# Performance work log

Measured on AMD Instinct MI355X. Metric: run time of the kernel, lower is better.

The kernel has to match this reference:

```python
import jax, jax.numpy as jnp
import numpy as np

K = 12  # kNN neighbors (includes self, as in PyG knn(x, x, k))
EPS = 1e-5


def bn(h, g, b):
    # Training-mode BatchNorm over all axes except the last (feature) axis.
    ax = tuple(range(h.ndim - 1))
    m = h.mean(axis=ax, keepdims=True)
    v = h.var(axis=ax, keepdims=True)  # biased variance, as BN uses
    return g * (h - m) * jax.lax.rsqrt(v + EPS) + b


def edge_conv(x, W1, b1, g, be, W2, b2):
    # x: [B, N, C] -> [B, N, H]. Dynamic kNN graph in feature space per graph.
    d2 = jnp.sum(x * x, axis=-1)                                  # [B, N]
    dist = d2[:, :, None] + d2[:, None, :] - 2.0 * jnp.einsum('bic,bjc->bij', x, x)
    _, idx = jax.lax.top_k(-dist, K)                              # [B, N, K]
    xj = jnp.take_along_axis(x[:, None, :, :], idx[:, :, :, None], axis=2)  # [B,N,K,C]
    xi = jnp.broadcast_to(x[:, :, None, :], xj.shape)
    e = jnp.concatenate([xi, xj - xi], axis=-1)                   # [B,N,K,2C]
    h = jax.nn.relu(bn(jnp.einsum('bnkc,ch->bnkh', e, W1) + b1, g, be))
    h = jnp.einsum('bnkh,ho->bnko', h, W2) + b2
    return h.mean(axis=2)                                         # mean aggr over K


def setup_inputs() -> dict:
    key = jax.random.key(0)
    ks = jax.random.split(key, 8)
    B, N, C, H, Hf, O = 32, 1024, 3, 64, 32, 2
    s = 0.1
    return {
        'x': jax.random.normal(ks[0], (B, N, C), jnp.float32),
        'w0a': jax.random.normal(ks[1], (2 * C, H), jnp.float32) * s,
        'b0a': jnp.zeros((H,), jnp.float32),
        'g0': jnp.ones((H,), jnp.float32),
        'be0': jnp.zeros((H,), jnp.float32),
        'w0b': jax.random.normal(ks[2], (H, H), jnp.float32) * s,
        'b0b': jnp.zeros((H,), jnp.float32),
        'wa': jax.random.normal(ks[3], (3, 2 * H, H), jnp.float32) * s,
        'ba': jnp.zeros((3, H), jnp.float32),
        'ga': jnp.ones((3, H), jnp.float32),
        'bea': jnp.zeros((3, H), jnp.float32),
        'wb': jax.random.normal(ks[4], (3, H, H), jnp.float32) * s,
        'bb': jnp.zeros((3, H), jnp.float32),
        'wf1': jax.random.normal(ks[5], (H, Hf), jnp.float32) * s,
        'bf1': jnp.zeros((Hf,), jnp.float32),
        'gf': jnp.ones((Hf,), jnp.float32),
        'bef': jnp.zeros((Hf,), jnp.float32),
        'wf2': jax.random.normal(ks[6], (Hf, O), jnp.float32) * s,
        'bf2': jnp.zeros((O,), jnp.float32),
    }


def reference(x, w0a, b0a, g0, be0, w0b, b0b, wa, ba, ga, bea, wb, bb,
              wf1, bf1, gf, bef, wf2, bf2):
    # Layer 0: input channels = 3
    h = edge_conv(x, w0a, b0a, g0, be0, w0b, b0b)
    # Layers 1..3: input channels = hidden
    for i in range(3):
        h = edge_conv(h, wa[i], ba[i], ga[i], bea[i], wb[i], bb[i])
    pooled = h.mean(axis=1)  # global_mean_pool over nodes -> [B, H]
    z = jax.nn.relu(bn(pooled @ wf1 + bf1, gf, bef))
    return z @ wf2 + bf2     # [B, 2]
```

## Files before the change

kernel.cpp:

```cpp
#include <hip/hip_runtime.h>
#include <cstddef>

#define BATCH 32
#define NPTS  1024
#define K_NN  12
#define HID   64
#define BN_EPS 1e-5f

typedef short bf16x8 __attribute__((ext_vector_type(8)));
typedef float f32x4 __attribute__((ext_vector_type(4)));

__device__ __forceinline__ unsigned long long dkey(float dval, int j) {
  int di = __float_as_int(dval);
  unsigned m = (unsigned)(di >> 31) | 0x80000000u;
  unsigned u = (unsigned)di ^ m;
  return ((unsigned long long)u << 32) | (unsigned)j;
}

__device__ __forceinline__ void cas_u64(unsigned long long &a, unsigned long long &b) {
  unsigned long long x = a, y = b;
  bool c = y < x;
  a = c ? y : x;
  b = c ? x : y;
}

__device__ __forceinline__ void sort16_u64(unsigned long long (&k)[16]) {
  cas_u64(k[0],k[1]);  cas_u64(k[2],k[3]);  cas_u64(k[4],k[5]);  cas_u64(k[6],k[7]);
  cas_u64(k[8],k[9]);  cas_u64(k[10],k[11]); cas_u64(k[12],k[13]); cas_u64(k[14],k[15]);
  cas_u64(k[0],k[2]);  cas_u64(k[1],k[3]);  cas_u64(k[4],k[6]);  cas_u64(k[5],k[7]);
  cas_u64(k[8],k[10]); cas_u64(k[9],k[11]); cas_u64(k[12],k[14]); cas_u64(k[13],k[15]);
  cas_u64(k[1],k[2]);  cas_u64(k[5],k[6]);  cas_u64(k[9],k[10]); cas_u64(k[13],k[14]);
  cas_u64(k[0],k[4]);  cas_u64(k[1],k[5]);  cas_u64(k[2],k[6]);  cas_u64(k[3],k[7]);
  cas_u64(k[8],k[12]); cas_u64(k[9],k[13]); cas_u64(k[10],k[14]); cas_u64(k[11],k[15]);
  cas_u64(k[2],k[4]);  cas_u64(k[3],k[5]);  cas_u64(k[10],k[12]); cas_u64(k[11],k[13]);
  cas_u64(k[1],k[2]);  cas_u64(k[3],k[4]);  cas_u64(k[5],k[6]);
  cas_u64(k[9],k[10]); cas_u64(k[11],k[12]); cas_u64(k[13],k[14]);
  cas_u64(k[0],k[8]);  cas_u64(k[1],k[9]);  cas_u64(k[2],k[10]); cas_u64(k[3],k[11]);
  cas_u64(k[4],k[12]); cas_u64(k[5],k[13]); cas_u64(k[6],k[14]); cas_u64(k[7],k[15]);
  cas_u64(k[4],k[8]);  cas_u64(k[5],k[9]);  cas_u64(k[6],k[10]); cas_u64(k[7],k[11]);
  cas_u64(k[2],k[4]);  cas_u64(k[3],k[5]);  cas_u64(k[6],k[8]);  cas_u64(k[7],k[9]);
  cas_u64(k[10],k[12]); cas_u64(k[11],k[13]);
  cas_u64(k[1],k[2]);  cas_u64(k[3],k[4]);  cas_u64(k[5],k[6]);  cas_u64(k[7],k[8]);
  cas_u64(k[9],k[10]); cas_u64(k[11],k[12]); cas_u64(k[13],k[14]);
}

__device__ __forceinline__ void merge12_u64(unsigned long long (&L)[12],
                                            const unsigned long long* S) {
#pragma unroll
  for (int i = 0; i < 12; ++i) {
    unsigned long long s = S[11 - i];
    L[i] = L[i] < s ? L[i] : s;
  }
  cas_u64(L[0],L[8]);  cas_u64(L[1],L[9]);  cas_u64(L[2],L[10]); cas_u64(L[3],L[11]);
  cas_u64(L[4],L[8]);  cas_u64(L[5],L[9]);  cas_u64(L[6],L[10]); cas_u64(L[7],L[11]);
  cas_u64(L[0],L[2]);  cas_u64(L[1],L[3]);  cas_u64(L[4],L[6]);  cas_u64(L[5],L[7]);
  cas_u64(L[8],L[10]); cas_u64(L[9],L[11]);
  cas_u64(L[0],L[1]);  cas_u64(L[2],L[3]);  cas_u64(L[4],L[5]);  cas_u64(L[6],L[7]);
  cas_u64(L[8],L[9]);  cas_u64(L[10],L[11]);
}

__global__ __launch_bounds__(512, 2) void knn64_mfma_kernel(
    const unsigned short* __restrict__ xh, const unsigned short* __restrict__ xm,
    const unsigned short* __restrict__ xl, const float* __restrict__ d2,
    int* __restrict__ idx,
    const float* __restrict__ hxi, const float* __restrict__ hxj,
    float* __restrict__ partial) {
  const int b    = blockIdx.y;
  const int lane = threadIdx.x & 63;
  const int wv_u = __builtin_amdgcn_readfirstlane(threadIdx.x >> 6);
  const int i0   = blockIdx.x * 64;
  const size_t bbase = (size_t)b * NPTS;
  const float* d2b = d2 + bbase;

  constexpr int NE = 8 * K_NN;
  __shared__ __align__(16) char smem[60416];
  unsigned short* alds = (unsigned short*)smem;
  float* slab = (float*)(smem + 25600 + wv_u * 4352);
  unsigned long long* lk = (unsigned long long*)smem;
  int* jlds = (int*)(smem + 49664);
  float* red1 = (float*)smem;
  float* red2 = (float*)(smem + 2048);

  const int qr = lane >> 4;
  const int lr = lane & 15;

  for (int it = threadIdx.x; it < 1536; it += 512) {
    const int row = it / 24, rem = it % 24, pl = rem >> 3, seg = rem & 7;
    const unsigned short* src = (pl == 0) ? xh : ((pl == 1) ? xm : xl);
    *(bf16x8*)(alds + row * 200 + pl * 64 + seg * 8) =
        *(const bf16x8*)(src + (bbase + i0 + row) * HID + seg * 8);
  }
  __syncthreads();

  unsigned long long L[K_NN];
#pragma unroll
  for (int k = 0; k < K_NN; ++k) L[k] = ~0ULL;

  const int j0 = wv_u * 128;

  bf16x8 Bh0, Bh1, Bm0, Bm1, Bl0, Bl1;
  {
    const size_t brow = (bbase + j0 + lr) * HID;
    Bh0 = *(const bf16x8*)(xh + brow + 0  + qr * 8);
    Bh1 = *(const bf16x8*)(xh + brow + 32 + qr * 8);
    Bm0 = *(const bf16x8*)(xm + brow + 0  + qr * 8);
    Bm1 = *(const bf16x8*)(xm + brow + 32 + qr * 8);
    Bl0 = *(const bf16x8*)(xl + brow + 0  + qr * 8);
    Bl1 = *(const bf16x8*)(xl + brow + 32 + qr * 8);
  }

#pragma unroll 1
  for (int chunk = 0; chunk < 8; ++chunk) {
    const int jb = j0 + chunk * 16;
    const bf16x8 bh0 = Bh0, bh1 = Bh1, bm0 = Bm0, bm1 = Bm1, bl0 = Bl0, bl1 = Bl1;

    f32x4 acc[4];
#pragma unroll
    for (int isub = 0; isub < 4; ++isub) acc[isub] = f32x4{0.f, 0.f, 0.f, 0.f};

#pragma unroll
    for (int isub = 0; isub < 4; ++isub) {
      const int ar = (isub * 16 + lr) * 200;
      bf16x8 Ah0 = *(const bf16x8*)(alds + ar + 0   + qr * 8);
      bf16x8 Ah1 = *(const bf16x8*)(alds + ar + 32  + qr * 8);
      bf16x8 Am0 = *(const bf16x8*)(alds + ar + 64  + qr * 8);
      bf16x8 Am1 = *(const bf16x8*)(alds + ar + 96  + qr * 8);
      bf16x8 Al0 = *(const bf16x8*)(alds + ar + 128 + qr * 8);
      bf16x8 Al1 = *(const bf16x8*)(alds + ar + 160 + qr * 8);
      f32x4 a = acc[isub];
      a = __builtin_amdgcn_mfma_f32_16x16x32_bf16(Ah0, bh0, a, 0, 0, 0);
      a = __builtin_amdgcn_mfma_f32_16x16x32_bf16(Ah1, bh1, a, 0, 0, 0);
      a = __builtin_amdgcn_mfma_f32_16x16x32_bf16(Ah0, bm0, a, 0, 0, 0);
      a = __builtin_amdgcn_mfma_f32_16x16x32_bf16(Ah1, bm1, a, 0, 0, 0);
      a = __builtin_amdgcn_mfma_f32_16x16x32_bf16(Am0, bh0, a, 0, 0, 0);
      a = __builtin_amdgcn_mfma_f32_16x16x32_bf16(Am1, bh1, a, 0, 0, 0);
      a = __builtin_amdgcn_mfma_f32_16x16x32_bf16(Ah0, bl0, a, 0, 0, 0);
      a = __builtin_amdgcn_mfma_f32_16x16x32_bf16(Ah1, bl1, a, 0, 0, 0);
      a = __builtin_amdgcn_mfma_f32_16x16x32_bf16(Al0, bh0, a, 0, 0, 0);
      a = __builtin_amdgcn_mfma_f32_16x16x32_bf16(Al1, bh1, a, 0, 0, 0);
      a = __builtin_amdgcn_mfma_f32_16x16x32_bf16(Am0, bm0, a, 0, 0, 0);
      a = __builtin_amdgcn_mfma_f32_16x16x32_bf16(Am1, bm1, a, 0, 0, 0);
      acc[isub] = a;
    }

    if (chunk < 7) {
      const size_t nrow = (bbase + jb + 16 + lr) * HID;
      Bh0 = *(const bf16x8*)(xh + nrow + 0  + qr * 8);
      Bh1 = *(const bf16x8*)(xh + nrow + 32 + qr * 8);
      Bm0 = *(const bf16x8*)(xm + nrow + 0  + qr * 8);
      Bm1 = *(const bf16x8*)(xm + nrow + 32 + qr * 8);
      Bl0 = *(const bf16x8*)(xl + nrow + 0  + qr * 8);
      Bl1 = *(const bf16x8*)(xl + nrow + 32 + qr * 8);
    }

#pragma unroll
    for (int isub = 0; isub < 4; ++isub)
#pragma unroll
      for (int r = 0; r < 4; ++r)
        slab[(isub * 16 + qr * 4 + r) * 17 + lr] = acc[isub][r];

    unsigned long long S[16];
#pragma unroll
    for (int jj = 0; jj < 16; ++jj) {
      const int j = jb + jj;
      const float dot = slab[lane * 17 + jj];
      const float dval = fmaf(-2.f, dot, d2b[j]);
      S[jj] = dkey(dval, j);
    }
    sort16_u64(S);
    merge12_u64(L, S);
  }

  __syncthreads();
#pragma unroll
  for (int k = 0; k < K_NN; ++k)
    lk[lane * (NE + 1) + wv_u * K_NN + k] = L[k];
  __syncthreads();

  unsigned long long Lm[K_NN];
  if (wv_u < 2) {
    if (wv_u == 0) {
#pragma unroll
      for (int k = 0; k < K_NN; ++k) Lm[k] = L[k];
    } else {
#pragma unroll
      for (int k = 0; k < K_NN; ++k) Lm[k] = lk[lane * (NE + 1) + 4 * K_NN + k];
    }
#pragma unroll 1
    for (int w = 1; w < 4; ++w) {
      unsigned long long M[K_NN];
#pragma unroll
      for (int k = 0; k < K_NN; ++k)
        M[k] = lk[lane * (NE + 1) + (wv_u * 4 + w) * K_NN + k];
      merge12_u64(Lm, M);
    }
  }
  __syncthreads();
  if (wv_u == 1) {
#pragma unroll
    for (int k = 0; k < K_NN; ++k) lk[lane * (NE + 1) + 4 * K_NN + k] = Lm[k];
  }
  __syncthreads();
  if (wv_u == 0) {
    unsigned long long M[K_NN];
#pragma unroll
    for (int k = 0; k < K_NN; ++k) M[k] = lk[lane * (NE + 1) + 4 * K_NN + k];
    merge12_u64(Lm, M);
    int* op = idx + ((size_t)b * NPTS + i0 + lane) * K_NN;
#pragma unroll
    for (int k = 0; k < K_NN; ++k) {
      int jv = (int)(unsigned)(Lm[k] & 0xFFFFFFFFu);
      op[k] = jv;
      jlds[lane * K_NN + k] = jv;
    }
  }
  __syncthreads();

  {
    const float* hxib = hxi + (bbase + i0) * HID;
    const float* hxjb = hxj + bbase * HID;
    float s1 = 0.f, s2 = 0.f;
#pragma unroll 1
    for (int t = 0; t < 8; ++t) {
      const int nl = wv_u * 8 + t;
      const float hv = hxib[(size_t)nl * HID + lane];
      int jj[K_NN];
#pragma unroll
      for (int k = 0; k < K_NN; ++k) jj[k] = jlds[nl * K_NN + k];
      float v[K_NN];
#pragma unroll
      for (int k = 0; k < K_NN; ++k) v[k] = hxjb[(size_t)jj[k] * HID + lane];
#pragma unroll
      for (int k = 0; k < K_NN; ++k) {
        float h = hv + v[k];
        s1 += h;
        s2 = fmaf(h, h, s2);
      }
    }
    red1[wv_u * HID + lane] = s1;
    red2[wv_u * HID + lane] = s2;
  }
  __syncthreads();
  if (threadIdx.x < 128) {
    const int f = threadIdx.x & 63;
    const float* r = (threadIdx.x < 64) ? red1 : red2;
    float a = 0.f;
#pragma unroll
    for (int w = 0; w < 8; ++w) a += r[w * HID + f];
    partial[((size_t)b * 16 + blockIdx.x) * 128 + threadIdx.x] = a;
  }
}

__global__ __launch_bounds__(512, 4) void knn3_kernel(
    const float* __restrict__ x, const float* __restrict__ d2,
    int* __restrict__ idx,
    const float* __restrict__ hxi, const float* __restrict__ hxj,
    float* __restrict__ partial) {
  const int b    = blockIdx.y;
  const int lane = threadIdx.x & 63;
  const int wv_u = __builtin_amdgcn_readfirstlane(threadIdx.x >> 6);
  const int i0   = blockIdx.x * 64;
  const int i    = i0 + lane;
  const size_t bbase = (size_t)b * NPTS;
  const float* xb  = x  + bbase * 3;
  const float* d2b = d2 + bbase;

  __shared__ __align__(16) char smem[27648];
  unsigned long long* buf = (unsigned long long*)smem;
  int* jlds = (int*)(smem + 24576);
  float* red1 = (float*)smem;
  float* red2 = (float*)(smem + 2048);

  float xi0 = xb[(size_t)i * 3 + 0];
  float xi1 = xb[(size_t)i * 3 + 1];
  float xi2v = xb[(size_t)i * 3 + 2];

  unsigned long long L[K_NN];
#pragma unroll
  for (int k = 0; k < K_NN; ++k) L[k] = ~0ULL;

  const int j0 = wv_u * 128;
#pragma unroll 1
  for (int ch = 0; ch < 8; ++ch) {
    unsigned long long S[16];
#pragma unroll
    for (int jj = 0; jj < 16; ++jj) {
      const int j = j0 + ch * 16 + jj;
      const float* xj = xb + (size_t)j * 3;
      const float d2j = d2b[j];
      float dot = fmaf(xi0, xj[0], 0.f);
      dot = fmaf(xi1, xj[1], dot);
      dot = fmaf(xi2v, xj[2], dot);
      S[jj] = dkey(fmaf(-2.f, dot, d2j), j);
    }
    sort16_u64(S);
    merge12_u64(L, S);
  }

  if (wv_u >= 4) {
#pragma unroll
    for (int k = 0; k < K_NN; ++k)
      buf[((wv_u - 4) * 64 + lane) * K_NN + k] = L[k];
  }
  __syncthreads();
  if (wv_u < 4) {
    unsigned long long M[K_NN];
#pragma unroll
    for (int k = 0; k < K_NN; ++k) M[k] = buf[(wv_u * 64 + lane) * K_NN + k];
    merge12_u64(L, M);
  }
  __syncthreads();
  if (wv_u == 2 || wv_u == 3) {
#pragma unroll
    for (int k = 0; k < K_NN; ++k)
      buf[((wv_u - 2) * 64 + lane) * K_NN + k] = L[k];
  }
  __syncthreads();
  if (wv_u < 2) {
    unsigned long long M[K_NN];
#pragma unroll
    for (int k = 0; k < K_NN; ++k) M[k] = buf[(wv_u * 64 + lane) * K_NN + k];
    merge12_u64(L, M);
  }
  __syncthreads();
  if (wv_u == 1) {
#pragma unroll
    for (int k = 0; k < K_NN; ++k) buf[lane * K_NN + k] = L[k];
  }
  __syncthreads();
  if (wv_u == 0) {
    unsigned long long M[K_NN];
#pragma unroll
    for (int k = 0; k < K_NN; ++k) M[k] = buf[lane * K_NN + k];
    merge12_u64(L, M);
    int* op = idx + ((size_t)b * NPTS + i0 + lane) * K_NN;
#pragma unroll
    for (int k = 0; k < K_NN; ++k) {
      int jv = (int)(unsigned)(L[k] & 0xFFFFFFFFu);
      op[k] = jv;
      jlds[lane * K_NN + k] = jv;
    }
  }
  __syncthreads();

  {
    const float* hxib = hxi + (bbase + i0) * HID;
    const float* hxjb2 = hxj + bbase * HID;
    float s1 = 0.f, s2 = 0.f;
#pragma unroll 1
    for (int t = 0; t < 8; ++t) {
      const int nl = wv_u * 8 + t;
      const float hv = hxib[(size_t)nl * HID + lane];
      int jj[K_NN];
#pragma unroll
      for (int k = 0; k < K_NN; ++k) jj[k] = jlds[nl * K_NN + k];
      float v[K_NN];
#pragma unroll
      for (int k = 0; k < K_NN; ++k) v[k] = hxjb2[(size_t)jj[k] * HID + lane];
#pragma unroll
      for (int k = 0; k < K_NN; ++k) {
        float h = hv + v[k];
        s1 += h;
        s2 = fmaf(h, h, s2);
      }
    }
    red1[wv_u * HID + lane] = s1;
    red2[wv_u * HID + lane] = s2;
  }
  __syncthreads();
  if (threadIdx.x < 128) {
    const int f = threadIdx.x & 63;
    const float* r = (threadIdx.x < 64) ? red1 : red2;
    float a = 0.f;
#pragma unroll
    for (int w = 0; w < 8; ++w) a += r[w * HID + f];
    partial[((size_t)b * 16 + blockIdx.x) * 128 + threadIdx.x] = a;
  }
}

__global__ __launch_bounds__(256) void rowgemm2_kernel(
    const float* __restrict__ X, const float* __restrict__ waL,
    const float* __restrict__ biasA,
    float* __restrict__ YA, float* __restrict__ YB) {
  __shared__ float wsa[HID * HID];
  __shared__ float wsb[HID * HID];
  for (int t = threadIdx.x; t < HID * HID; t += 256) {
    float wbv = waL[4096 + t];
    wsa[t] = waL[t] - wbv;
    wsb[t] = wbv;
  }
  __syncthreads();

  const int lane = threadIdx.x & 63;
  const int wv   = threadIdx.x >> 6;
  const int fq   = lane & 15;
  const int rg   = lane >> 4;
  const int r0   = blockIdx.x * 32 + wv * 8 + rg * 2;

  const float4* X4 = (const float4*)X;
  const float4* WA4 = (const float4*)wsa;
  const float4* WB4 = (const float4*)wsb;
  float aA0[4] = {0,0,0,0}, aA1[4] = {0,0,0,0};
  float aB0[4] = {0,0,0,0}, aB1[4] = {0,0,0,0};

#pragma unroll 2
  for (int cq = 0; cq < 16; ++cq) {
    float4 xa = X4[(size_t)r0 * 16 + cq];
    float4 xb_ = X4[(size_t)(r0 + 1) * 16 + cq];
    float ea[4] = {xa.x, xa.y, xa.z, xa.w};
    float eb[4] = {xb_.x, xb_.y, xb_.z, xb_.w};
#pragma unroll
    for (int d = 0; d < 4; ++d) {
      float4 wa4 = WA4[(cq * 4 + d) * 16 + fq];
      float4 wb4 = WB4[(cq * 4 + d) * 16 + fq];
      float wA[4] = {wa4.x, wa4.y, wa4.z, wa4.w};
      float wB[4] = {wb4.x, wb4.y, wb4.z, wb4.w};
#pragma unroll
      for (int k = 0; k < 4; ++k) {
        aA0[k] = fmaf(ea[d], wA[k], aA0[k]);
        aA1[k] = fmaf(eb[d], wA[k], aA1[k]);
        aB0[k] = fmaf(ea[d], wB[k], aB0[k]);
        aB1[k] = fmaf(eb[d], wB[k], aB1[k]);
      }
    }
  }
  float4 b4 = ((const float4*)biasA)[fq];
  float4 oA0{aA0[0] + b4.x, aA0[1] + b4.y, aA0[2] + b4.z, aA0[3] + b4.w};
  float4 oA1{aA1[0] + b4.x, aA1[1] + b4.y, aA1[2] + b4.z, aA1[3] + b4.w};
  float4 oB0{aB0[0], aB0[1], aB0[2], aB0[3]};
  float4 oB1{aB1[0], aB1[1], aB1[2], aB1[3]};
  ((float4*)YA)[(size_t)r0 * 16 + fq] = oA0;
  ((float4*)YA)[(size_t)(r0 + 1) * 16 + fq] = oA1;
  ((float4*)YB)[(size_t)r0 * 16 + fq] = oB0;
  ((float4*)YB)[(size_t)(r0 + 1) * 16 + fq] = oB1;
}

__global__ __launch_bounds__(256) void dual3_kernel(
    const float* __restrict__ x, const float* __restrict__ w0a,
    const float* __restrict__ b1,
    float* __restrict__ hxi, float* __restrict__ hxj,
    float* __restrict__ d2out) {
  __shared__ float Cs[3 * HID], Bs[3 * HID], bs[HID];
  for (int t = threadIdx.x; t < 3 * HID; t += 256) {
    float bv = w0a[192 + t];
    Cs[t] = w0a[t] - bv;
    Bs[t] = bv;
  }
  if (threadIdx.x < HID) bs[threadIdx.x] = b1[threadIdx.x];
  __syncthreads();

  const int lane = threadIdx.x & 63;
  const int wv   = __builtin_amdgcn_readfirstlane(threadIdx.x >> 6);
  const int node0 = blockIdx.x * 32;
#pragma unroll 1
  for (int it = 0; it < 8; ++it) {
    const int n = node0 + it * 4 + wv;
    const float* xr = x + (size_t)n * 3;
    float x0 = xr[0], x1 = xr[1], x2 = xr[2];
    float hi = bs[lane];
    hi = fmaf(x0, Cs[0 * HID + lane], hi);
    hi = fmaf(x1, Cs[1 * HID + lane], hi);
    hi = fmaf(x2, Cs[2 * HID + lane], hi);
    float hj = x0 * Bs[0 * HID + lane];
    hj = fmaf(x1, Bs[1 * HID + lane], hj);
    hj = fmaf(x2, Bs[2 * HID + lane], hj);
    hxi[(size_t)n * HID + lane] = hi;
    hxj[(size_t)n * HID + lane] = hj;
    if (lane == 0)
      d2out[n] = fmaf(x0, x0, fmaf(x1, x1, x2 * x2));
  }
}

__global__ __launch_bounds__(256) void egapply_gemm_kernel(
    const int* __restrict__ idx, const float* __restrict__ hxi,
    const float* __restrict__ hxj, const float* __restrict__ partial,
    const float* __restrict__ g, const float* __restrict__ be,
    const float* __restrict__ W2, const float* __restrict__ b2,
    float* __restrict__ out, float* __restrict__ d2out,
    unsigned short* __restrict__ xsh, unsigned short* __restrict__ xsm,
    unsigned short* __restrict__ xsl, float* __restrict__ pooled) {
  __shared__ float w2s[HID * HID];
  __shared__ float red[32][HID];
  __shared__ float sAB[128];
  for (int t = threadIdx.x; t < HID * HID; t += 256) w2s[t] = W2[t];

  const int lane = threadIdx.x & 63;
  const int wv   = __builtin_amdgcn_readfirstlane(threadIdx.x >> 6);
  const int node0 = blockIdx.x * 32;

  {
    const int t    = threadIdx.x & 127;
    const int half = threadIdx.x >> 7;
    float a0 = 0.f, a1 = 0.f, a2 = 0.f, a3 = 0.f;
    const int gb0 = half * 256;
    for (int gb = gb0; gb < gb0 + 256; gb += 4) {
      a0 += partial[(size_t)(gb + 0) * 128 + t];
      a1 += partial[(size_t)(gb + 1) * 128 + t];
      a2 += partial[(size_t)(gb + 2) * 128 + t];
      a3 += partial[(size_t)(gb + 3) * 128 + t];
    }
    float* sm = &red[0][0];
    sm[half * 128 + t] = (a0 + a1) + (a2 + a3);
    __syncthreads();
    if (threadIdx.x < 128) sm[256 + t] = sm[t] + sm[128 + t];
    __syncthreads();
    if (threadIdx.x < HID) {
      const float inv_n = 1.f / (float)(BATCH * NPTS * K_NN);
      float m = sm[256 + threadIdx.x] * inv_n;
      float v = sm[256 + HID + threadIdx.x] * inv_n - m * m;
      float A = g[threadIdx.x] * rsqrtf(v + BN_EPS);
      sAB[threadIdx.x] = A;
      sAB[HID + threadIdx.x] = be[threadIdx.x] - m * A;
    }
    __syncthreads();
  }
  const float A = sAB[lane], Bc = sAB[HID + lane];

#pragma unroll 1
  for (int it = 0; it < 4; ++it) {
    const int n0 = node0 + it * 8 + wv;
    const int n1 = n0 + 4;
    const int bbase = (n0 >> 10) << 10;
    const int* ip0 = idx + (size_t)n0 * K_NN;
    const int* ip1 = idx + (size_t)n1 * K_NN;
    int j0[K_NN], j1[K_NN];
#pragma unroll
    for (int k = 0; k < K_NN; ++k) { j0[k] = ip0[k]; j1[k] = ip1[k]; }
    const float hv0 = hxi[(size_t)n0 * HID + lane];
    const float hv1 = hxi[(size_t)n1 * HID + lane];
    float v0[K_NN], v1[K_NN];
#pragma unroll
    for (int k = 0; k < K_NN; ++k) {
      v0[k] = hxj[(size_t)(bbase + j0[k]) * HID + lane];
      v1[k] = hxj[(size_t)(bbase + j1[k]) * HID + lane];
    }
    float a0 = 0.f, a1 = 0.f;
#pragma unroll
    for (int k = 0; k < K_NN; ++k) {
      a0 += fmaxf(fmaf(A, hv0 + v0[k], Bc), 0.f);
      a1 += fmaxf(fmaf(A, hv1 + v1[k], Bc), 0.f);
    }
    red[it * 8 + wv][lane] = a0;
    red[it * 8 + 4 + wv][lane] = a1;
  }
  __syncthreads();

  const float b2f = b2[lane];
  const float inv = 1.f / (float)K_NN;
  float psum = 0.f;
#pragma unroll 2
  for (int p = 0; p < 8; ++p) {
    int rr = p * 4 + wv;
    float acc0 = 0.f, acc1 = 0.f;
#pragma unroll 8
    for (int h = 0; h < HID; h += 2) {
      acc0 = fmaf(red[rr][h],     w2s[h * HID + lane],       acc0);
      acc1 = fmaf(red[rr][h + 1], w2s[(h + 1) * HID + lane], acc1);
    }
    float val = fmaf(acc0 + acc1, inv, b2f);
    const size_t o = (size_t)(node0 + rr) * HID + lane;
    out[o] = val;
    psum += val;

    unsigned u = __float_as_uint(val);
    unsigned short hh = (unsigned short)((u + 0x7FFFu + ((u >> 16) & 1u)) >> 16);
    float r1 = val - __uint_as_float((unsigned)hh << 16);
    unsigned ur = __float_as_uint(r1);
    unsigned short mm = (unsigned short)((ur + 0x7FFFu + ((ur >> 16) & 1u)) >> 16);
    float r2 = r1 - __uint_as_float((unsigned)mm << 16);
    unsigned ur2 = __float_as_uint(r2);
    unsigned short ll = (unsigned short)((ur2 + 0x7FFFu + ((ur2 >> 16) & 1u)) >> 16);
    xsh[o] = hh; xsm[o] = mm; xsl[o] = ll;

    float sq = val * val;
#pragma unroll
    for (int off = 1; off < 64; off <<= 1) sq += __shfl_xor(sq, off, 64);
    if (lane == 0) d2out[node0 + rr] = sq;
  }

  if (pooled != nullptr) {
    __syncthreads();
    red[wv][lane] = psum;
    __syncthreads();
    if (threadIdx.x < HID) {
      const int bb = node0 >> 10;
      float s = (red[0][lane] + red[1][lane]) + (red[2][lane] + red[3][lane]);
      atomicAdd(&pooled[bb * HID + lane], s * (1.f / (float)NPTS));
    }
  }
}

__global__ __launch_bounds__(256) void head_kernel(const float* __restrict__ pooled,
    const float* __restrict__ wf1, const float* __restrict__ bf1,
    const float* __restrict__ gf, const float* __restrict__ bef,
    const float* __restrict__ wf2, const float* __restrict__ bf2,
    float* __restrict__ out) {
  __shared__ float pl[BATCH * HID];
  __shared__ float t[BATCH * 32];
  __shared__ float Ab[32], Bb[32];
  for (int i = threadIdx.x; i < BATCH * HID; i += 256) pl[i] = pooled[i];
  __syncthreads();
  for (int i = threadIdx.x; i < BATCH * 32; i += 256) {
    int s = i >> 5, f1 = i & 31;
    float acc = bf1[f1];
    for (int h = 0; h < HID; ++h) acc = fmaf(pl[s * HID + h], wf1[h * 32 + f1], acc);
    t[i] = acc;
  }
  __syncthreads();
  if (threadIdx.x < 32) {
    int f1 = threadIdx.x;
    float m = 0.f;
    for (int s = 0; s < BATCH; ++s) m += t[s * 32 + f1];
    m *= (1.f / (float)BATCH);
    float v = 0.f;
    for (int s = 0; s < BATCH; ++s) { float d = t[s * 32 + f1] - m; v = fmaf(d, d, v); }
    v *= (1.f / (float)BATCH);
    float A = gf[f1] * rsqrtf(v + BN_EPS);
    Ab[f1] = A; Bb[f1] = bef[f1] - m * A;
  }
  __syncthreads();
  for (int i = threadIdx.x; i < BATCH * 32; i += 256) {
    int f1 = i & 31;
    t[i] = fmaxf(fmaf(Ab[f1], t[i], Bb[f1]), 0.f);
  }
  __syncthreads();
  if (threadIdx.x < BATCH * 2) {
    int s = threadIdx.x >> 1, o = threadIdx.x & 1;
    float acc = bf2[o];
    for (int f1 = 0; f1 < 32; ++f1) acc = fmaf(t[s * 32 + f1], wf2[f1 * 2 + o], acc);
    out[s * 2 + o] = acc;
  }
}

extern "C" void kernel_launch(void* const* d_in, const int* in_sizes, int n_in,
                              void* d_out, int out_size, void* d_ws, size_t ws_size,
                              hipStream_t stream) {
  const float* x   = (const float*)d_in[0];
  const float* w0a = (const float*)d_in[1];
  const float* b0a = (const float*)d_in[2];
  const float* g0  = (const float*)d_in[3];
  const float* be0 = (const float*)d_in[4];
  const float* w0b = (const float*)d_in[5];
  const float* b0b = (const float*)d_in[6];
  const float* wa  = (const float*)d_in[7];
  const float* ba  = (const float*)d_in[8];
  const float* ga  = (const float*)d_in[9];
  const float* bea = (const float*)d_in[10];
  const float* wb  = (const float*)d_in[11];
  const float* bb  = (const float*)d_in[12];
  const float* wf1 = (const float*)d_in[13];
  const float* bf1 = (const float*)d_in[14];
  const float* gf  = (const float*)d_in[15];
  const float* bef = (const float*)d_in[16];
  const float* wf2 = (const float*)d_in[17];
  const float* bf2 = (const float*)d_in[18];

  float* ws = (float*)d_ws;
  const size_t HN = (size_t)BATCH * NPTS * HID;
  const size_t ROWS = (size_t)BATCH * NPTS;
  float* bufA    = ws;
  float* bufB    = bufA + HN;
  float* hxi     = bufB + HN;
  float* hxjb    = hxi + HN;
  int*   idxb    = (int*)(hxjb + HN);
  float* d2buf   = (float*)(idxb + ROWS * K_NN);
  float* stats   = d2buf + ROWS;
  float* partial = stats + 256;
  float* pooled  = partial + 1024 * 128;
  unsigned short* xsh = (unsigned short*)(pooled + 2048);
  unsigned short* xsm = xsh + HN;
  unsigned short* xsl = xsm + HN;

  hipMemsetAsync(pooled, 0, BATCH * HID * sizeof(float), stream);

  dual3_kernel<<<1024, 256, 0, stream>>>(x, w0a, b0a, hxi, hxjb, d2buf);
  knn3_kernel<<<dim3(16, BATCH), 512, 0, stream>>>(x, d2buf, idxb, hxi, hxjb, partial);
  egapply_gemm_kernel<<<1024, 256, 0, stream>>>(idxb, hxi, hxjb, partial, g0, be0,
                                                w0b, b0b, bufA, d2buf,
                                                xsh, xsm, xsl, nullptr);

  const float* cur = bufA;
  float* nxt = bufB;
  for (int i = 0; i < 3; ++i) {
    rowgemm2_kernel<<<(int)(ROWS / 32), 256, 0, stream>>>(cur, wa + (size_t)i * 8192,
                                                          ba + i * HID, hxi, hxjb);
    knn64_mfma_kernel<<<dim3(16, BATCH), 512, 0, stream>>>(xsh, xsm, xsl, d2buf, idxb,
                                                           hxi, hxjb, partial);
    egapply_gemm_kernel<<<1024, 256, 0, stream>>>(idxb, hxi, hxjb, partial,
                                                  ga + i * HID, bea + i * HID,
                                                  wb + (size_t)i * 4096, bb + i * HID,
                                                  nxt, d2buf, xsh, xsm, xsl,
                                                  (i == 2) ? pooled : nullptr);
    const float* t = cur; cur = nxt; nxt = (float*)t;
  }

  head_kernel<<<1, 256, 0, stream>>>(pooled, wf1, bf1, gf, bef, wf2, bf2, (float*)d_out);
}
```

Before: 498.3 us.

## Fuse next-layer row GEMM into egapply and hoist BN stat reduction

```diff
diff --git a/kernel.cpp b/kernel.cpp
--- a/kernel.cpp
+++ b/kernel.cpp
@@ -378,63 +378,6 @@
   }
 }
 
-__global__ __launch_bounds__(256) void rowgemm2_kernel(
-    const float* __restrict__ X, const float* __restrict__ waL,
-    const float* __restrict__ biasA,
-    float* __restrict__ YA, float* __restrict__ YB) {
-  __shared__ float wsa[HID * HID];
-  __shared__ float wsb[HID * HID];
-  for (int t = threadIdx.x; t < HID * HID; t += 256) {
-    float wbv = waL[4096 + t];
-    wsa[t] = waL[t] - wbv;
-    wsb[t] = wbv;
-  }
-  __syncthreads();
-
-  const int lane = threadIdx.x & 63;
-  const int wv   = threadIdx.x >> 6;
-  const int fq   = lane & 15;
-  const int rg   = lane >> 4;
-  const int r0   = blockIdx.x * 32 + wv * 8 + rg * 2;
-
-  const float4* X4 = (const float4*)X;
-  const float4* WA4 = (const float4*)wsa;
-  const float4* WB4 = (const float4*)wsb;
-  float aA0[4] = {0,0,0,0}, aA1[4] = {0,0,0,0};
-  float aB0[4] = {0,0,0,0}, aB1[4] = {0,0,0,0};
-
-#pragma unroll 2
-  for (int cq = 0; cq < 16; ++cq) {
-    float4 xa = X4[(size_t)r0 * 16 + cq];
-    float4 xb_ = X4[(size_t)(r0 + 1) * 16 + cq];
-    float ea[4] = {xa.x, xa.y, xa.z, xa.w};
-    float eb[4] = {xb_.x, xb_.y, xb_.z, xb_.w};
-#pragma unroll
-    for (int d = 0; d < 4; ++d) {
-      float4 wa4 = WA4[(cq * 4 + d) * 16 + fq];
-      float4 wb4 = WB4[(cq * 4 + d) * 16 + fq];
-      float wA[4] = {wa4.x, wa4.y, wa4.z, wa4.w};
-      float wB[4] = {wb4.x, wb4.y, wb4.z, wb4.w};
-#pragma unroll
-      for (int k = 0; k < 4; ++k) {
-        aA0[k] = fmaf(ea[d], wA[k], aA0[k]);
-        aA1[k] = fmaf(eb[d], wA[k], aA1[k]);
-        aB0[k] = fmaf(ea[d], wB[k], aB0[k]);
-        aB1[k] = fmaf(eb[d], wB[k], aB1[k]);
-      }
-    }
-  }
-  float4 b4 = ((const float4*)biasA)[fq];
-  float4 oA0{aA0[0] + b4.x, aA0[1] + b4.y, aA0[2] + b4.z, aA0[3] + b4.w};
-  float4 oA1{aA1[0] + b4.x, aA1[1] + b4.y, aA1[2] + b4.z, aA1[3] + b4.w};
-  float4 oB0{aB0[0], aB0[1], aB0[2], aB0[3]};
-  float4 oB1{aB1[0], aB1[1], aB1[2], aB1[3]};
-  ((float4*)YA)[(size_t)r0 * 16 + fq] = oA0;
-  ((float4*)YA)[(size_t)(r0 + 1) * 16 + fq] = oA1;
-  ((float4*)YB)[(size_t)r0 * 16 + fq] = oB0;
-  ((float4*)YB)[(size_t)(r0 + 1) * 16 + fq] = oB1;
-}
-
 __global__ __launch_bounds__(256) void dual3_kernel(
     const float* __restrict__ x, const float* __restrict__ w0a,
     const float* __restrict__ b1,
@@ -471,50 +414,53 @@
   }
 }
 
+__global__ __launch_bounds__(512) void bn_reduce_finalize_kernel(
+    const float* __restrict__ g, const float* __restrict__ be,
+    const float* __restrict__ partial, float* __restrict__ stats) {
+  const int t   = threadIdx.x & 127;
+  const int grp = threadIdx.x >> 7;
+  float a0 = 0.f, a1 = 0.f, a2 = 0.f, a3 = 0.f;
+  const int gb0 = grp * 128;
+  for (int gb = gb0; gb < gb0 + 128; gb += 4) {
+    a0 += partial[(size_t)(gb + 0) * 128 + t];
+    a1 += partial[(size_t)(gb + 1) * 128 + t];
+    a2 += partial[(size_t)(gb + 2) * 128 + t];
+    a3 += partial[(size_t)(gb + 3) * 128 + t];
+  }
+  __shared__ float sm[4][128];
+  sm[grp][t] = (a0 + a1) + (a2 + a3);
+  __syncthreads();
+  if (threadIdx.x < 128)
+    sm[0][t] = (sm[0][t] + sm[1][t]) + (sm[2][t] + sm[3][t]);
+  __syncthreads();
+  if (threadIdx.x < HID) {
+    const float inv_n = 1.f / (float)(BATCH * NPTS * K_NN);
+    float m = sm[0][t] * inv_n;
+    float v = sm[0][HID + t] * inv_n - m * m;
+    float A = g[t] * rsqrtf(v + BN_EPS);
+    stats[128 + t] = A;
+    stats[192 + t] = be[t] - m * A;
+  }
+}
+
 __global__ __launch_bounds__(256) void egapply_gemm_kernel(
     const int* __restrict__ idx, const float* __restrict__ hxi,
-    const float* __restrict__ hxj, const float* __restrict__ partial,
-    const float* __restrict__ g, const float* __restrict__ be,
+    const float* __restrict__ hxj, const float* __restrict__ stats,
     const float* __restrict__ W2, const float* __restrict__ b2,
-    float* __restrict__ out, float* __restrict__ d2out,
+    float* __restrict__ d2out,
     unsigned short* __restrict__ xsh, unsigned short* __restrict__ xsm,
-    unsigned short* __restrict__ xsl, float* __restrict__ pooled) {
+    unsigned short* __restrict__ xsl,
+    const float* __restrict__ waL, const float* __restrict__ biasA,
+    float* __restrict__ hxi_out, float* __restrict__ hxj_out,
+    float* __restrict__ pooled) {
   __shared__ float w2s[HID * HID];
   __shared__ float red[32][HID];
-  __shared__ float sAB[128];
   for (int t = threadIdx.x; t < HID * HID; t += 256) w2s[t] = W2[t];
 
   const int lane = threadIdx.x & 63;
   const int wv   = __builtin_amdgcn_readfirstlane(threadIdx.x >> 6);
   const int node0 = blockIdx.x * 32;
-
-  {
-    const int t    = threadIdx.x & 127;
-    const int half = threadIdx.x >> 7;
-    float a0 = 0.f, a1 = 0.f, a2 = 0.f, a3 = 0.f;
-    const int gb0 = half * 256;
-    for (int gb = gb0; gb < gb0 + 256; gb += 4) {
-      a0 += partial[(size_t)(gb + 0) * 128 + t];
-      a1 += partial[(size_t)(gb + 1) * 128 + t];
-      a2 += partial[(size_t)(gb + 2) * 128 + t];
-      a3 += partial[(size_t)(gb + 3) * 128 + t];
-    }
-    float* sm = &red[0][0];
-    sm[half * 128 + t] = (a0 + a1) + (a2 + a3);
-    __syncthreads();
-    if (threadIdx.x < 128) sm[256 + t] = sm[t] + sm[128 + t];
-    __syncthreads();
-    if (threadIdx.x < HID) {
-      const float inv_n = 1.f / (float)(BATCH * NPTS * K_NN);
-      float m = sm[256 + threadIdx.x] * inv_n;
-      float v = sm[256 + HID + threadIdx.x] * inv_n - m * m;
-      float A = g[threadIdx.x] * rsqrtf(v + BN_EPS);
-      sAB[threadIdx.x] = A;
-      sAB[HID + threadIdx.x] = be[threadIdx.x] - m * A;
-    }
-    __syncthreads();
-  }
-  const float A = sAB[lane], Bc = sAB[HID + lane];
+  const float A = stats[128 + lane], Bc = stats[192 + lane];
 
 #pragma unroll 1
   for (int it = 0; it < 4; ++it) {
@@ -547,6 +493,7 @@
 
   const float b2f = b2[lane];
   const float inv = 1.f / (float)K_NN;
+  float vals[8];
   float psum = 0.f;
 #pragma unroll 2
   for (int p = 0; p < 8; ++p) {
@@ -558,9 +505,9 @@
       acc1 = fmaf(red[rr][h + 1], w2s[(h + 1) * HID + lane], acc1);
     }
     float val = fmaf(acc0 + acc1, inv, b2f);
+    vals[p] = val;
+    psum += val;
     const size_t o = (size_t)(node0 + rr) * HID + lane;
-    out[o] = val;
-    psum += val;
 
     unsigned u = __float_as_uint(val);
     unsigned short hh = (unsigned short)((u + 0x7FFFu + ((u >> 16) & 1u)) >> 16);
@@ -576,6 +523,35 @@
 #pragma unroll
     for (int off = 1; off < 64; off <<= 1) sq += __shfl_xor(sq, off, 64);
     if (lane == 0) d2out[node0 + rr] = sq;
+  }
+
+  if (waL != nullptr) {
+    __syncthreads();
+#pragma unroll
+    for (int p = 0; p < 8; ++p) red[p * 4 + wv][lane] = vals[p];
+    __syncthreads();
+#pragma unroll 1
+    for (int phase = 0; phase < 2; ++phase) {
+      for (int t = threadIdx.x; t < HID * HID; t += 256) {
+        float wbv = waL[4096 + t];
+        w2s[t] = (phase == 0) ? (waL[t] - wbv) : wbv;
+      }
+      __syncthreads();
+      const float bias = (phase == 0) ? biasA[lane] : 0.f;
+      float* dst = (phase == 0) ? hxi_out : hxj_out;
+#pragma unroll 2
+      for (int p = 0; p < 8; ++p) {
+        int rr = p * 4 + wv;
+        float a0 = 0.f, a1 = 0.f;
+#pragma unroll 8
+        for (int h = 0; h < HID; h += 2) {
+          a0 = fmaf(red[rr][h],     w2s[h * HID + lane],       a0);
+          a1 = fmaf(red[rr][h + 1], w2s[(h + 1) * HID + lane], a1);
+        }
+        dst[(size_t)(node0 + rr) * HID + lane] = bias + a0 + a1;
+      }
+      __syncthreads();
+    }
   }
 
   if (pooled != nullptr) {
@@ -658,11 +634,11 @@
   float* ws = (float*)d_ws;
   const size_t HN = (size_t)BATCH * NPTS * HID;
   const size_t ROWS = (size_t)BATCH * NPTS;
-  float* bufA    = ws;
-  float* bufB    = bufA + HN;
-  float* hxi     = bufB + HN;
-  float* hxjb    = hxi + HN;
-  int*   idxb    = (int*)(hxjb + HN);
+  float* hxiA    = ws;
+  float* hxjA    = hxiA + HN;
+  float* hxiB    = hxjA + HN;
+  float* hxjB    = hxiB + HN;
+  int*   idxb    = (int*)(hxjB + HN);
   float* d2buf   = (float*)(idxb + ROWS * K_NN);
   float* stats   = d2buf + ROWS;
   float* partial = stats + 256;
@@ -673,25 +649,37 @@
 
   hipMemsetAsync(pooled, 0, BATCH * HID * sizeof(float), stream);
 
-  dual3_kernel<<<1024, 256, 0, stream>>>(x, w0a, b0a, hxi, hxjb, d2buf);
-  knn3_kernel<<<dim3(16, BATCH), 512, 0, stream>>>(x, d2buf, idxb, hxi, hxjb, partial);
-  egapply_gemm_kernel<<<1024, 256, 0, stream>>>(idxb, hxi, hxjb, partial, g0, be0,
-                                                w0b, b0b, bufA, d2buf,
-                                                xsh, xsm, xsl, nullptr);
-
-  const float* cur = bufA;
-  float* nxt = bufB;
+  float* hip[2] = {hxiA, hxiB};
+  float* hjp[2] = {hxjA, hxjB};
+
+  dual3_kernel<<<1024, 256, 0, stream>>>(x, w0a, b0a, hxiA, hxjA, d2buf);
+  knn3_kernel<<<dim3(16, BATCH), 512, 0, stream>>>(x, d2buf, idxb, hxiA, hxjA, partial);
+  bn_reduce_finalize_kernel<<<1, 512, 0, stream>>>(g0, be0, partial, stats);
+  egapply_gemm_kernel<<<1024, 256, 0, stream>>>(idxb, hxiA, hxjA, stats, w0b, b0b,
+                                                d2buf, xsh, xsm, xsl,
+                                                wa, ba, hxiB, hxjB, nullptr);
+
+  int cur = 1;
   for (int i = 0; i < 3; ++i) {
-    rowgemm2_kernel<<<(int)(ROWS / 32), 256, 0, stream>>>(cur, wa + (size_t)i * 8192,
-                                                          ba + i * HID, hxi, hxjb);
     knn64_mfma_kernel<<<dim3(16, BATCH), 512, 0, stream>>>(xsh, xsm, xsl, d2buf, idxb,
-                                                           hxi, hxjb, partial);
-    egapply_gemm_kernel<<<1024, 256, 0, stream>>>(idxb, hxi, hxjb, partial,
-                                                  ga + i * HID, bea + i * HID,
-                                                  wb + (size_t)i * 4096, bb + i * HID,
-                                                  nxt, d2buf, xsh, xsm, xsl,
-                                                  (i == 2) ? pooled : nullptr);
-    const float* t = cur; cur = nxt; nxt = (float*)t;
+                                                           hip[cur], hjp[cur], partial);
+    bn_reduce_finalize_kernel<<<1, 512, 0, stream>>>(ga + i * HID, bea + i * HID,
+                                                     partial, stats);
+    if (i < 2) {
+      egapply_gemm_kernel<<<1024, 256, 0, stream>>>(idxb, hip[cur], hjp[cur], stats,
+                                                    wb + (size_t)i * 4096, bb + i * HID,
+                                                    d2buf, xsh, xsm, xsl,
+                                                    wa + (size_t)(i + 1) * 8192,
+                                                    ba + (i + 1) * HID,
+                                                    hip[cur ^ 1], hjp[cur ^ 1], nullptr);
+    } else {
+      egapply_gemm_kernel<<<1024, 256, 0, stream>>>(idxb, hip[cur], hjp[cur], stats,
+                                                    wb + (size_t)i * 4096, bb + i * HID,
+                                                    d2buf, xsh, xsm, xsl,
+                                                    nullptr, nullptr, nullptr, nullptr,
+                                                    pooled);
+    }
+    cur ^= 1;
   }
 
   head_kernel<<<1, 256, 0, stream>>>(pooled, wf1, bf1, gf, bef, wf2, bf2, (float*)d_out);
```

Result: slower. 536.8 us (+7.7%).
